# Optimization experiments

Measured on AMD Instinct MI355X. Metric: run time of the kernel, lower is better.

Reference implementation:

```python
import jax, jax.numpy as jnp
import numpy as np

HEADS = 8
DIM_HEAD = 64
SCALE = DIM_HEAD ** -0.5
POS_DIM = 64


def _sincos_pe(H, W, dim, dtype):
    # matches build_2d_sincos_pos_embed: [1, dim, H, W]
    y = jnp.linspace(-1.0, 1.0, H)[:, None] * jnp.ones((1, W), jnp.float32)
    x = jnp.ones((H, 1), jnp.float32) * jnp.linspace(-1.0, 1.0, W)[None, :]
    omega = 1.0 / (10000.0 ** (jnp.arange(dim // 4, dtype=jnp.float32) / (dim // 4)))
    px = x[..., None] * omega  # [H, W, dim//4]
    py = y[..., None] * omega
    pe = jnp.concatenate([jnp.sin(px), jnp.cos(px), jnp.sin(py), jnp.cos(py)], axis=-1)
    return pe.transpose(2, 0, 1)[None].astype(dtype)


def _conv2d(x, w):
    return jax.lax.conv_general_dilated(
        x, w, (1, 1), 'SAME', dimension_numbers=('NCHW', 'OIHW', 'NCHW'))


def _sobel(d):
    kx = jnp.array([[1, 0, -1], [2, 0, -2], [1, 0, -1]], jnp.float32).reshape(1, 1, 3, 3)
    ky = jnp.array([[1, 2, 1], [0, 0, 0], [-1, -2, -1]], jnp.float32).reshape(1, 1, 3, 3)
    return _conv2d(d, kx), _conv2d(d, ky)


def setup_inputs() -> dict:
    key = jax.random.key(0)
    ks = jax.random.split(key, 8)
    B, C, H, W = 2, 256, 64, 64
    hid = HEADS * DIM_HEAD  # 512
    s = 0.02
    return {
        'x': jax.random.normal(ks[0], (B, C, H, W), jnp.float32),
        'dsm': jax.random.uniform(ks[1], (B, 1, H, W), jnp.float32),
        'wq': jax.random.normal(ks[2], (hid, C), jnp.float32) * s,
        'wkv': jax.random.normal(ks[3], (2 * hid, C + 1), jnp.float32) * s,
        'wout': jax.random.normal(ks[4], (C, hid), jnp.float32) * s,
        'bout': jnp.zeros((C,), jnp.float32),
        'w_hape': jax.random.normal(ks[5], (hid, POS_DIM + 3), jnp.float32) * s,
        'b_hape': jnp.zeros((hid,), jnp.float32),
        'w_alpha': jax.random.normal(ks[6], (1, 1, 3, 3), jnp.float32) * 0.1,
        'b_alpha': jnp.zeros((1,), jnp.float32),
    }


def reference(x, dsm, wq, wkv, wout, bout, w_hape, b_hape, w_alpha, b_alpha):
    B, C, H, W = x.shape
    hid = wq.shape[0]
    # per-sample min-max normalize DSM over spatial dims
    dmin = dsm.min(axis=(2, 3), keepdims=True)
    dmax = dsm.max(axis=(2, 3), keepdims=True)
    d = (dsm - dmin) / (dmax - dmin + 1e-6)
    # HAPE: [PE | h | grad_h] -> 1x1 conv to hidden
    pe = jnp.broadcast_to(_sincos_pe(H, W, POS_DIM, x.dtype), (B, POS_DIM, H, W))
    gx, gy = _sobel(d)
    hape_in = jnp.concatenate([pe, d, gx, gy], axis=1)  # [B, 67, H, W]
    hape_k = jnp.einsum('oc,bchw->bohw', w_hape, hape_in) + b_hape[None, :, None, None]
    # QKV via 1x1 convs
    q = jnp.einsum('oc,bchw->bohw', wq, x)
    kv = jnp.einsum('oc,bchw->bohw', wkv, jnp.concatenate([x, d], axis=1))
    k = kv[:, :hid] + hape_k
    v = kv[:, hid:]
    to_heads = lambda t: t.reshape(B, HEADS, DIM_HEAD, H * W)  # b (h c) x y -> b h c (xy)
    qh = to_heads(q) * SCALE
    kh = to_heads(k)
    vh = to_heads(v)
    sim = jnp.einsum('bhdi,bhdj->bhij', qh, kh)  # [B, h, N, N]
    attn = jax.nn.softmax(sim, axis=-1)
    out = jnp.einsum('bhij,bhdj->bhid', attn, vh)  # [B, h, N, d]
    # b h (x y) d -> b (h d) x y
    out = out.transpose(0, 1, 3, 2).reshape(B, HEADS * DIM_HEAD, H, W)
    out = jnp.einsum('oc,bchw->bohw', wout, out) + bout[None, :, None, None]
    # fine: gradient-magnitude alpha gating
    mag = jnp.sqrt(jnp.maximum(gx, 0.0) ** 2 + jnp.maximum(gy, 0.0) ** 2 + 1e-12)
    alpha = jax.nn.sigmoid(_conv2d(mag, w_alpha) + b_alpha[None, :, None, None])
    return x + out * alpha
```

## Files before the change

### kernel.cpp

```cpp
#include <hip/hip_runtime.h>
#include <math.h>

#define NPOS 4096
#define MTOT 8192
#define KP   352
#define HT 64
#define WT 64

typedef unsigned short ushortT;
typedef short v8s __attribute__((ext_vector_type(8)));
typedef float v4f __attribute__((ext_vector_type(4)));

static __device__ __forceinline__ ushortT bfr(float f) {
    union { float f; unsigned u; } v; v.f = f;
    return (ushortT)((v.u + 0x8000u) >> 16);
}
static __device__ __forceinline__ unsigned pack2bf(float a, float b) {
    union { float f; unsigned u; } ua, ub; ua.f = a; ub.f = b;
    return __builtin_amdgcn_perm(ub.u + 0x8000u, ua.u + 0x8000u, 0x07060302u);
}
static __device__ __forceinline__ unsigned pack2bf_t(float a, float b) {
    union { float f; unsigned u; } ua, ub; ua.f = a; ub.f = b;
    return __builtin_amdgcn_perm(ub.u, ua.u, 0x07060302u);
}
static __device__ __forceinline__ float fexp2(float x) {
#if __has_builtin(__builtin_amdgcn_exp2f)
    return __builtin_amdgcn_exp2f(x);
#else
    return exp2f(x);
#endif
}

__global__ void k_minmax(const float* __restrict__ dsm, float* __restrict__ mm) {
    int b = blockIdx.x;
    const float* p = dsm + (size_t)b * NPOS;
    float mn = 1e30f, mx = -1e30f;
    for (int i = threadIdx.x; i < NPOS; i += 256) {
        float v = p[i];
        mn = fminf(mn, v); mx = fmaxf(mx, v);
    }
    for (int off = 32; off; off >>= 1) {
        mn = fminf(mn, __shfl_xor(mn, off, 64));
        mx = fmaxf(mx, __shfl_xor(mx, off, 64));
    }
    __shared__ float smn[4], smx[4];
    int wid = threadIdx.x >> 6;
    if ((threadIdx.x & 63) == 0) { smn[wid] = mn; smx[wid] = mx; }
    __syncthreads();
    if (threadIdx.x == 0) {
        mn = fminf(fminf(smn[0], smn[1]), fminf(smn[2], smn[3]));
        mx = fmaxf(fmaxf(smx[0], smx[1]), fmaxf(smx[2], smx[3]));
        mm[b * 2 + 0] = mn; mm[b * 2 + 1] = mx;
    }
}

__global__ void k_prep(const float* __restrict__ dsm, const float* __restrict__ mm,
                       const float* __restrict__ walpha, const float* __restrict__ balpha,
                       ushortT* __restrict__ F, float* __restrict__ alpha) {
    int idx = blockIdx.x * 256 + threadIdx.x;
    int b = idx / NPOS, n = idx % NPOS;
    int hh = n / WT, ww = n % WT;
    float dmin = mm[b * 2], dmax = mm[b * 2 + 1];
    float inv = 1.0f / (dmax - dmin + 1e-6f);
    const float* dp = dsm + (size_t)b * NPOS;

    float dwin[5][5];
    #pragma unroll
    for (int dy = 0; dy < 5; dy++)
        #pragma unroll
        for (int dx = 0; dx < 5; dx++) {
            int y = hh + dy - 2, x = ww + dx - 2;
            float v = 0.0f;
            if (y >= 0 && y < HT && x >= 0 && x < WT) v = (dp[y * WT + x] - dmin) * inv;
            dwin[dy][dx] = v;
        }

    float gxc = 0.f, gyc = 0.f;
    float conv = 0.f;
    #pragma unroll
    for (int oy = 0; oy < 3; oy++)
        #pragma unroll
        for (int ox = 0; ox < 3; ox++) {
            int qy = hh + oy - 1, qx = ww + ox - 1;
            float m = 0.0f;
            if (qy >= 0 && qy < HT && qx >= 0 && qx < WT) {
                float gx = dwin[oy][ox] - dwin[oy][ox + 2]
                         + 2.f * dwin[oy + 1][ox] - 2.f * dwin[oy + 1][ox + 2]
                         + dwin[oy + 2][ox] - dwin[oy + 2][ox + 2];
                float gy = dwin[oy][ox] + 2.f * dwin[oy][ox + 1] + dwin[oy][ox + 2]
                         - dwin[oy + 2][ox] - 2.f * dwin[oy + 2][ox + 1] - dwin[oy + 2][ox + 2];
                if (oy == 1 && ox == 1) { gxc = gx; gyc = gy; }
                float rx = fmaxf(gx, 0.f), ry = fmaxf(gy, 0.f);
                m = sqrtf(rx * rx + ry * ry + 1e-12f);
            }
            conv += walpha[oy * 3 + ox] * m;
        }
    alpha[idx] = 1.f / (1.f + __expf(-(conv + balpha[0])));

    ushortT* fb = F + (size_t)idx * KP;
    fb[256] = bfr(dwin[2][2]);
    fb[257] = bfr(gxc);
    fb[258] = bfr(gyc);
    float xc = -1.f + 2.f * (float)ww / 63.f;
    float yc = -1.f + 2.f * (float)hh / 63.f;
    const float l2w = 13.287712379549449f;
    #pragma unroll
    for (int i = 0; i < 16; i++) {
        float omega = exp2f(-(float)i * (l2w / 16.f));
        float px = xc * omega, py = yc * omega;
        fb[259 + i]      = bfr(__sinf(px));
        fb[259 + 16 + i] = bfr(__cosf(px));
        fb[259 + 32 + i] = bfr(__sinf(py));
        fb[259 + 48 + i] = bfr(__cosf(py));
    }
    #pragma unroll
    for (int z = 323; z < KP; z++) fb[z] = 0;
}

__global__ void k_cast(const float* __restrict__ x, ushortT* __restrict__ F) {
    __shared__ __align__(16) ushortT Tl[64][72];
    int nt = blockIdx.x * 64;
    int b = blockIdx.y >> 2, ct = (blockIdx.y & 3) * 64;
    int t = threadIdx.x;
    #pragma unroll
    for (int rep = 0; rep < 4; rep++) {
        int row = rep * 16 + (t >> 4), c4 = (t & 15) * 4;
        float4 f4 = *(const float4*)&x[((size_t)(b * 256 + ct + row)) * NPOS + nt + c4];
        Tl[c4 + 0][row] = bfr(f4.x);
        Tl[c4 + 1][row] = bfr(f4.y);
        Tl[c4 + 2][row] = bfr(f4.z);
        Tl[c4 + 3][row] = bfr(f4.w);
    }
    __syncthreads();
    #pragma unroll
    for (int rep = 0; rep < 2; rep++) {
        int slot = rep * 256 + t, row = slot >> 3, c8 = slot & 7;
        *(uint4*)&F[((size_t)(b * 4096 + nt + row)) * KP + ct + c8 * 8] = *(uint4*)&Tl[row][c8 * 8];
    }
}

__global__ void k_wcprep(const float* __restrict__ wq, const float* __restrict__ wkv,
                         const float* __restrict__ whape, const float* __restrict__ bhape,
                         ushortT* __restrict__ Wc, float* __restrict__ biasc) {
    int idx = blockIdx.x * 256 + threadIdx.x;
    int o = idx / KP, k = idx % KP;
    float v = 0.f;
    if (o < 512) {
        if (k < 256) v = wq[o * 256 + k] * 0.18033688011112042f;
        if (k == 0) biasc[o] = 0.f;
    } else if (o < 1024) {
        int r = o - 512;
        if (k < 257) v = wkv[r * 257 + k];
        if (k == 256)      v += whape[r * 67 + 64];
        else if (k == 257) v = whape[r * 67 + 65];
        else if (k == 258) v = whape[r * 67 + 66];
        else if (k >= 259 && k < 323) v = whape[r * 67 + (k - 259)];
        if (k == 0) biasc[o] = bhape[r];
    } else {
        int r = o - 512;
        if (k < 257) v = wkv[r * 257 + k];
        if (k == 0) biasc[o] = 0.f;
    }
    Wc[idx] = bfr(v);
}

__global__ void k_wout(const float* __restrict__ wout, ushortT* __restrict__ woutb) {
    int idx = blockIdx.x * 256 + threadIdx.x;
    woutb[idx] = bfr(wout[idx]);
}

__global__ __launch_bounds__(256) void k_gemm1(const ushortT* __restrict__ Wc, const ushortT* __restrict__ F,
                                               const float* __restrict__ biasc,
                                               ushortT* __restrict__ qT, ushortT* __restrict__ kT,
                                               ushortT* __restrict__ vv) {
    __shared__ __align__(16) ushortT Al[64][40];
    __shared__ __align__(16) ushortT Bl[64][40];
    __shared__ __align__(16) ushortT Vt[64][72];
    int mt = blockIdx.x * 64;
    int ot = blockIdx.y * 64;
    int t = threadIdx.x, w = t >> 6, lane = t & 63, u = lane & 15, quad = lane >> 4;
    int arow = t >> 2, ac8 = t & 3;
    v4f acc[4] = {};
    for (int k0 = 0; k0 < KP; k0 += 32) {
        __syncthreads();
        *(uint4*)&Al[arow][ac8 * 8] = *(const uint4*)&Wc[(size_t)(ot + arow) * KP + k0 + ac8 * 8];
        *(uint4*)&Bl[arow][ac8 * 8] = *(const uint4*)&F[(size_t)(mt + arow) * KP + k0 + ac8 * 8];
        __syncthreads();
        v8s a = *(v8s*)&Al[w * 16 + u][quad * 8];
        #pragma unroll
        for (int n4 = 0; n4 < 4; n4++) {
            v8s bb = *(v8s*)&Bl[n4 * 16 + u][quad * 8];
            acc[n4] = __builtin_amdgcn_mfma_f32_16x16x32_bf16(a, bb, acc[n4], 0, 0, 0);
        }
    }
    int obase = ot + w * 16 + quad * 4;
    float bo[4];
    #pragma unroll
    for (int r = 0; r < 4; r++) bo[r] = biasc[obase + r];
    if (ot < 1024) {
        int h = (ot >> 6) & 7;
        ushortT* dst = (ot < 512) ? qT : kT;
        #pragma unroll
        for (int n4 = 0; n4 < 4; n4++) {
            int m = mt + n4 * 16 + u;
            uint2 val;
            val.x = pack2bf(acc[n4][0] + bo[0], acc[n4][1] + bo[1]);
            val.y = pack2bf(acc[n4][2] + bo[2], acc[n4][3] + bo[3]);
            *(uint2*)&dst[((size_t)h * MTOT + m) * 64 + w * 16 + quad * 4] = val;
        }
    } else {
        __syncthreads();
        #pragma unroll
        for (int n4 = 0; n4 < 4; n4++) {
            int ml = n4 * 16 + u;
            #pragma unroll
            for (int r = 0; r < 4; r++) Vt[w * 16 + quad * 4 + r][ml] = bfr(acc[n4][r] + bo[r]);
        }
        __syncthreads();
        #pragma unroll
        for (int rep = 0; rep < 2; rep++) {
            int slot = rep * 256 + t, row = slot >> 3, c8 = slot & 7;
            *(uint4*)&vv[(size_t)(ot - 1024 + row) * MTOT + mt + c8 * 8] = *(uint4*)&Vt[row][c8 * 8];
        }
    }
}

#define LIDX(row, cb) (((row) << 6) + ((((cb) ^ ((row) & 7))) << 3))
__global__ __launch_bounds__(256, 2) void k_flash(const ushortT* __restrict__ qT,
                                                  const ushortT* __restrict__ kT,
                                                  const ushortT* __restrict__ vv,
                                                  float* __restrict__ Opart,
                                                  float* __restrict__ liPart) {
    __shared__ __align__(16) ushortT Kbuf[2][64 * 64];
    __shared__ __align__(16) ushortT Vbuf[2][64 * 64];
    __shared__ __align__(16) ushortT Pw[4][64 * 64];

    int it = blockIdx.x;
    int bh = blockIdx.y;
    int half = blockIdx.z;
    int b = bh >> 3, h = bh & 7;
    int colbase = b * NPOS;
    int t = threadIdx.x, w = t >> 6, lane = t & 63, u = lane & 15, quad = lane >> 4;
    int qb = it * 256 + w * 64;

    const ushortT* Qg = qT + ((size_t)h * MTOT + colbase + qb) * 64;
    const ushortT* Kg = kT + ((size_t)h * MTOT + colbase + half * 2048) * 64;
    const ushortT* Vg = vv + ((size_t)(h * 64)) * MTOT + colbase + half * 2048;
    ushortT* P = &Pw[w][0];

    int row0 = t >> 3,        c80 = t & 7;
    int row1 = (256 + t) >> 3, c81 = t & 7;

    v8s bq[4][2];
    #pragma unroll
    for (int g = 0; g < 4; g++)
        #pragma unroll
        for (int hf = 0; hf < 2; hf++)
            bq[g][hf] = *(const v8s*)&Qg[(size_t)(g * 16 + u) * 64 + hf * 32 + quad * 8];

    float li[4] = {0.f, 0.f, 0.f, 0.f};
    v4f O[4][4] = {};

    uint4 kr0 = *(const uint4*)&Kg[(size_t)row0 * 64 + c80 * 8];
    uint4 kr1 = *(const uint4*)&Kg[(size_t)row1 * 64 + c81 * 8];
    uint4 vr0 = *(const uint4*)&Vg[(size_t)row0 * MTOT + c80 * 8];
    uint4 vr1 = *(const uint4*)&Vg[(size_t)row1 * MTOT + c81 * 8];

    for (int jc = 0; jc < 32; jc++) {
        int cur = jc & 1;
        *(uint4*)&Kbuf[cur][LIDX(row0, c80)] = kr0;
        *(uint4*)&Kbuf[cur][LIDX(row1, c81)] = kr1;
        *(uint4*)&Vbuf[cur][LIDX(row0, c80)] = vr0;
        *(uint4*)&Vbuf[cur][LIDX(row1, c81)] = vr1;
        if (jc + 1 < 32) {
            int jb = (jc + 1) * 64;
            kr0 = *(const uint4*)&Kg[(size_t)(jb + row0) * 64 + c80 * 8];
            kr1 = *(const uint4*)&Kg[(size_t)(jb + row1) * 64 + c81 * 8];
            vr0 = *(const uint4*)&Vg[(size_t)row0 * MTOT + jb + c80 * 8];
            vr1 = *(const uint4*)&Vg[(size_t)row1 * MTOT + jb + c81 * 8];
        }
        __syncthreads();

        const ushortT* Kb = &Kbuf[cur][0];
        const ushortT* Vb = &Vbuf[cur][0];

        #pragma unroll
        for (int k4 = 0; k4 < 4; k4++) {
            v8s ak0 = *(const v8s*)&Kb[LIDX(k4 * 16 + u, quad)];
            v8s ak1 = *(const v8s*)&Kb[LIDX(k4 * 16 + u, 4 + quad)];
            v4f st[4];
            #pragma unroll
            for (int g = 0; g < 4; g++) {
                st[g] = (v4f){0.f, 0.f, 0.f, 0.f};
                st[g] = __builtin_amdgcn_mfma_f32_16x16x32_bf16(ak0, bq[g][0], st[g], 0, 0, 0);
                st[g] = __builtin_amdgcn_mfma_f32_16x16x32_bf16(ak1, bq[g][1], st[g], 0, 0, 0);
            }
            #pragma unroll
            for (int g = 0; g < 4; g++) {
                float p0 = fexp2(st[g][0]);
                float p1 = fexp2(st[g][1]);
                float p2 = fexp2(st[g][2]);
                float p3 = fexp2(st[g][3]);
                li[g] += (p0 + p1) + (p2 + p3);
                uint2 pv; pv.x = pack2bf_t(p0, p1); pv.y = pack2bf_t(p2, p3);
                *(uint2*)&P[LIDX(g * 16 + u, k4 * 2 + (quad >> 1)) + (quad & 1) * 4] = pv;
            }
        }

        v8s bp[4][2];
        #pragma unroll
        for (int g = 0; g < 4; g++)
            #pragma unroll
            for (int ks = 0; ks < 2; ks++)
                bp[g][ks] = *(v8s*)&P[LIDX(g * 16 + u, ks * 4 + quad)];
        #pragma unroll
        for (int d4 = 0; d4 < 4; d4++) {
            v8s av0 = *(const v8s*)&Vb[LIDX(d4 * 16 + u, quad)];
            v8s av1 = *(const v8s*)&Vb[LIDX(d4 * 16 + u, 4 + quad)];
            #pragma unroll
            for (int g = 0; g < 4; g++) {
                O[d4][g] = __builtin_amdgcn_mfma_f32_16x16x32_bf16(av0, bp[g][0], O[d4][g], 0, 0, 0);
                O[d4][g] = __builtin_amdgcn_mfma_f32_16x16x32_bf16(av1, bp[g][1], O[d4][g], 0, 0, 0);
            }
        }
    }

    #pragma unroll
    for (int g = 0; g < 4; g++) {
        li[g] += __shfl_xor(li[g], 16, 64);
        li[g] += __shfl_xor(li[g], 32, 64);
        int q = qb + g * 16 + u;
        size_t m2 = (size_t)(half * 2 + b) * 4096 + q;
        size_t base = m2 * 512 + h * 64;
        #pragma unroll
        for (int d4 = 0; d4 < 4; d4++) {
            float4 o4;
            o4.x = O[d4][g][0]; o4.y = O[d4][g][1]; o4.z = O[d4][g][2]; o4.w = O[d4][g][3];
            *(float4*)&Opart[base + d4 * 16 + quad * 4] = o4;
        }
        if (quad == 0) liPart[m2 * 8 + h] = li[g];
    }
}

__global__ __launch_bounds__(256) void k_comb(const float* __restrict__ Opart,
                                              const float* __restrict__ liPart,
                                              ushortT* __restrict__ aoB) {
    int tid = blockIdx.x * 256 + threadIdx.x;
    int m = tid >> 7, c4 = (tid & 127) * 4, h = c4 >> 6;
    float l = liPart[(size_t)m * 8 + h] + liPart[(size_t)(8192 + m) * 8 + h];
    float inv = 1.f / l;
    float4 o0 = *(const float4*)&Opart[(size_t)m * 512 + c4];
    float4 o1 = *(const float4*)&Opart[(size_t)(8192 + m) * 512 + c4];
    uint2 val;
    val.x = pack2bf((o0.x + o1.x) * inv, (o0.y + o1.y) * inv);
    val.y = pack2bf((o0.z + o1.z) * inv, (o0.w + o1.w) * inv);
    *(uint2*)&aoB[(size_t)m * 512 + c4] = val;
}

__global__ __launch_bounds__(256) void k_gemm2(const ushortT* __restrict__ woutb, const ushortT* __restrict__ aoB,
                                               const float* __restrict__ bout, const float* __restrict__ x,
                                               const float* __restrict__ alpha, float* __restrict__ out) {
    __shared__ __align__(16) ushortT Al[64][40];
    __shared__ __align__(16) ushortT Bl[64][40];
    int mt = blockIdx.x * 64;
    int ot = blockIdx.y * 64;
    int t = threadIdx.x, w = t >> 6, lane = t & 63, u = lane & 15, quad = lane >> 4;
    int arow = t >> 2, ac8 = t & 3;
    v4f acc[4] = {};
    for (int k0 = 0; k0 < 512; k0 += 32) {
        __syncthreads();
        *(uint4*)&Al[arow][ac8 * 8] = *(const uint4*)&woutb[(size_t)(ot + arow) * 512 + k0 + ac8 * 8];
        *(uint4*)&Bl[arow][ac8 * 8] = *(const uint4*)&aoB[(size_t)(mt + arow) * 512 + k0 + ac8 * 8];
        __syncthreads();
        v8s a = *(v8s*)&Al[w * 16 + u][quad * 8];
        #pragma unroll
        for (int n4 = 0; n4 < 4; n4++) {
            v8s bb = *(v8s*)&Bl[n4 * 16 + u][quad * 8];
            acc[n4] = __builtin_amdgcn_mfma_f32_16x16x32_bf16(a, bb, acc[n4], 0, 0, 0);
        }
    }
    int b = mt >> 12, n0 = mt & 4095;
    int obase = ot + w * 16 + quad * 4;
    float bo[4];
    #pragma unroll
    for (int r = 0; r < 4; r++) bo[r] = bout[obase + r];
    #pragma unroll
    for (int n4 = 0; n4 < 4; n4++) {
        int n = n0 + n4 * 16 + u;
        float al = alpha[(size_t)b * NPOS + n];
        #pragma unroll
        for (int r = 0; r < 4; r++) {
            size_t xi = ((size_t)(b * 256 + obase + r)) * NPOS + n;
            out[xi] = x[xi] + (acc[n4][r] + bo[r]) * al;
        }
    }
}

extern "C" void kernel_launch(void* const* d_in, const int* in_sizes, int n_in,
                              void* d_out, int out_size, void* d_ws, size_t ws_size,
                              hipStream_t stream) {
    const float* x      = (const float*)d_in[0];
    const float* dsm    = (const float*)d_in[1];
    const float* wq     = (const float*)d_in[2];
    const float* wkv    = (const float*)d_in[3];
    const float* wout   = (const float*)d_in[4];
    const float* bout   = (const float*)d_in[5];
    const float* whape  = (const float*)d_in[6];
    const float* bhape  = (const float*)d_in[7];
    const float* walpha = (const float*)d_in[8];
    const float* balpha = (const float*)d_in[9];
    float* out = (float*)d_out;
    float* ws  = (float*)d_ws;

    size_t off = 0;
    float* mm    = ws + off; off += 256;
    float* alpha = ws + off; off += (size_t)2 * NPOS;
    float* biasc = ws + off; off += 2048;
    float* Opart  = ws + off; off += (size_t)2 * MTOT * 512;
    float* liPart = ws + off; off += (size_t)2 * MTOT * 8;
    ushortT* F     = (ushortT*)(ws + off); off += (size_t)MTOT * KP / 2;
    ushortT* Wc    = (ushortT*)(ws + off); off += (size_t)1536 * KP / 2;
    ushortT* woutb = (ushortT*)(ws + off); off += (size_t)256 * 512 / 2;
    ushortT* qT    = (ushortT*)(ws + off); off += (size_t)8 * MTOT * 64 / 2;
    ushortT* kT    = (ushortT*)(ws + off); off += (size_t)8 * MTOT * 64 / 2;
    ushortT* vv    = (ushortT*)(ws + off); off += (size_t)512 * MTOT / 2;
    ushortT* aoB   = (ushortT*)(ws + off); off += (size_t)MTOT * 512 / 2;
    (void)in_sizes; (void)n_in; (void)out_size; (void)ws_size;

    k_minmax<<<2, 256, 0, stream>>>(dsm, mm);
    k_prep<<<32, 256, 0, stream>>>(dsm, mm, walpha, balpha, F, alpha);
    k_cast<<<dim3(64, 8), 256, 0, stream>>>(x, F);
    k_wcprep<<<(1536 * KP) / 256, 256, 0, stream>>>(wq, wkv, whape, bhape, Wc, biasc);
    k_wout<<<512, 256, 0, stream>>>(wout, woutb);
    k_gemm1<<<dim3(128, 24), 256, 0, stream>>>(Wc, F, biasc, qT, kT, vv);
    k_flash<<<dim3(16, 16, 2), 256, 0, stream>>>(qT, kT, vv, Opart, liPart);
    k_comb<<<4096, 256, 0, stream>>>(Opart, liPart, aoB);
    k_gemm2<<<dim3(128, 4), 256, 0, stream>>>(woutb, aoB, bout, x, alpha, out);
}
```

Measured before the change: 214.3 us.

## Shuffle P via permlane swaps, drop LDS staging, split keys four ways

The P tile (exp scores) is no longer written to and re-read from shared memory. It is packed in registers and moved into the MFMA B-operand layout with permlane32/permlane16 swap instructions. Removing the P buffer halves the kernel's shared memory, so launch bounds are raised to 4 blocks per CU, and the key range is split four ways instead of two to launch more blocks. The combine kernel now sums four partials, which doubles the fp32 partial-output traffic, and the tighter register budget at higher occupancy risks spills.

```diff
diff --git a/kernel.cpp b/kernel.cpp
--- a/kernel.cpp
+++ b/kernel.cpp
@@ -6,10 +6,14 @@
 #define KP   352
 #define HT 64
 #define WT 64
+#define NSPLIT 4
+#define KEYS_PER (NPOS / NSPLIT)
+#define NCH (KEYS_PER / 64)
 
 typedef unsigned short ushortT;
 typedef short v8s __attribute__((ext_vector_type(8)));
 typedef float v4f __attribute__((ext_vector_type(4)));
+typedef unsigned uint2v __attribute__((ext_vector_type(2)));
 
 static __device__ __forceinline__ ushortT bfr(float f) {
     union { float f; unsigned u; } v; v.f = f;
@@ -226,14 +230,13 @@
 }
 
 #define LIDX(row, cb) (((row) << 6) + ((((cb) ^ ((row) & 7))) << 3))
-__global__ __launch_bounds__(256, 2) void k_flash(const ushortT* __restrict__ qT,
+__global__ __launch_bounds__(256, 4) void k_flash(const ushortT* __restrict__ qT,
                                                   const ushortT* __restrict__ kT,
                                                   const ushortT* __restrict__ vv,
                                                   float* __restrict__ Opart,
                                                   float* __restrict__ liPart) {
     __shared__ __align__(16) ushortT Kbuf[2][64 * 64];
     __shared__ __align__(16) ushortT Vbuf[2][64 * 64];
-    __shared__ __align__(16) ushortT Pw[4][64 * 64];
 
     int it = blockIdx.x;
     int bh = blockIdx.y;
@@ -244,9 +247,8 @@
     int qb = it * 256 + w * 64;
 
     const ushortT* Qg = qT + ((size_t)h * MTOT + colbase + qb) * 64;
-    const ushortT* Kg = kT + ((size_t)h * MTOT + colbase + half * 2048) * 64;
-    const ushortT* Vg = vv + ((size_t)(h * 64)) * MTOT + colbase + half * 2048;
-    ushortT* P = &Pw[w][0];
+    const ushortT* Kg = kT + ((size_t)h * MTOT + colbase + half * KEYS_PER) * 64;
+    const ushortT* Vg = vv + ((size_t)(h * 64)) * MTOT + colbase + half * KEYS_PER;
 
     int row0 = t >> 3,        c80 = t & 7;
     int row1 = (256 + t) >> 3, c81 = t & 7;
@@ -266,13 +268,13 @@
     uint4 vr0 = *(const uint4*)&Vg[(size_t)row0 * MTOT + c80 * 8];
     uint4 vr1 = *(const uint4*)&Vg[(size_t)row1 * MTOT + c81 * 8];
 
-    for (int jc = 0; jc < 32; jc++) {
+    for (int jc = 0; jc < NCH; jc++) {
         int cur = jc & 1;
         *(uint4*)&Kbuf[cur][LIDX(row0, c80)] = kr0;
         *(uint4*)&Kbuf[cur][LIDX(row1, c81)] = kr1;
         *(uint4*)&Vbuf[cur][LIDX(row0, c80)] = vr0;
         *(uint4*)&Vbuf[cur][LIDX(row1, c81)] = vr1;
-        if (jc + 1 < 32) {
+        if (jc + 1 < NCH) {
             int jb = (jc + 1) * 64;
             kr0 = *(const uint4*)&Kg[(size_t)(jb + row0) * 64 + c80 * 8];
             kr1 = *(const uint4*)&Kg[(size_t)(jb + row1) * 64 + c81 * 8];
@@ -284,6 +286,7 @@
         const ushortT* Kb = &Kbuf[cur][0];
         const ushortT* Vb = &Vbuf[cur][0];
 
+        unsigned pk0[4][4], pk1[4][4];
         #pragma unroll
         for (int k4 = 0; k4 < 4; k4++) {
             v8s ak0 = *(const v8s*)&Kb[LIDX(k4 * 16 + u, quad)];
@@ -302,17 +305,26 @@
                 float p2 = fexp2(st[g][2]);
                 float p3 = fexp2(st[g][3]);
                 li[g] += (p0 + p1) + (p2 + p3);
-                uint2 pv; pv.x = pack2bf_t(p0, p1); pv.y = pack2bf_t(p2, p3);
-                *(uint2*)&P[LIDX(g * 16 + u, k4 * 2 + (quad >> 1)) + (quad & 1) * 4] = pv;
+                pk0[g][k4] = pack2bf_t(p0, p1);
+                pk1[g][k4] = pack2bf_t(p2, p3);
             }
         }
 
         v8s bp[4][2];
         #pragma unroll
-        for (int g = 0; g < 4; g++)
+        for (int g = 0; g < 4; g++) {
             #pragma unroll
-            for (int ks = 0; ks < 2; ks++)
-                bp[g][ks] = *(v8s*)&P[LIDX(g * 16 + u, ks * 4 + quad)];
+            for (int ks = 0; ks < 2; ks++) {
+                uint2v r0 = __builtin_amdgcn_permlane32_swap(pk0[g][2 * ks], pk0[g][2 * ks + 1], false, false);
+                uint2v r1 = __builtin_amdgcn_permlane32_swap(pk1[g][2 * ks], pk1[g][2 * ks + 1], false, false);
+                uint2v t0 = __builtin_amdgcn_permlane16_swap(r0.x, r0.y, false, false);
+                uint2v t1 = __builtin_amdgcn_permlane16_swap(r1.x, r1.y, false, false);
+                union { uint4 u4; v8s s; } cv;
+                cv.u4.x = t0.x; cv.u4.y = t1.x; cv.u4.z = t0.y; cv.u4.w = t1.y;
+                bp[g][ks] = cv.s;
+            }
+        }
+
         #pragma unroll
         for (int d4 = 0; d4 < 4; d4++) {
             v8s av0 = *(const v8s*)&Vb[LIDX(d4 * 16 + u, quad)];
@@ -347,13 +359,19 @@
                                               ushortT* __restrict__ aoB) {
     int tid = blockIdx.x * 256 + threadIdx.x;
     int m = tid >> 7, c4 = (tid & 127) * 4, h = c4 >> 6;
-    float l = liPart[(size_t)m * 8 + h] + liPart[(size_t)(8192 + m) * 8 + h];
+    float l = 0.f;
+    #pragma unroll
+    for (int s = 0; s < NSPLIT; s++) l += liPart[((size_t)s * 8192 + m) * 8 + h];
     float inv = 1.f / l;
-    float4 o0 = *(const float4*)&Opart[(size_t)m * 512 + c4];
-    float4 o1 = *(const float4*)&Opart[(size_t)(8192 + m) * 512 + c4];
+    float ox = 0.f, oy = 0.f, oz = 0.f, ow = 0.f;
+    #pragma unroll
+    for (int s = 0; s < NSPLIT; s++) {
+        float4 o = *(const float4*)&Opart[((size_t)s * 8192 + m) * 512 + c4];
+        ox += o.x; oy += o.y; oz += o.z; ow += o.w;
+    }
     uint2 val;
-    val.x = pack2bf((o0.x + o1.x) * inv, (o0.y + o1.y) * inv);
-    val.y = pack2bf((o0.z + o1.z) * inv, (o0.w + o1.w) * inv);
+    val.x = pack2bf(ox * inv, oy * inv);
+    val.y = pack2bf(oz * inv, ow * inv);
     *(uint2*)&aoB[(size_t)m * 512 + c4] = val;
 }
 
@@ -416,8 +434,8 @@
     float* mm    = ws + off; off += 256;
     float* alpha = ws + off; off += (size_t)2 * NPOS;
     float* biasc = ws + off; off += 2048;
-    float* Opart  = ws + off; off += (size_t)2 * MTOT * 512;
-    float* liPart = ws + off; off += (size_t)2 * MTOT * 8;
+    float* Opart  = ws + off; off += (size_t)NSPLIT * MTOT * 512;
+    float* liPart = ws + off; off += (size_t)NSPLIT * MTOT * 8;
     ushortT* F     = (ushortT*)(ws + off); off += (size_t)MTOT * KP / 2;
     ushortT* Wc    = (ushortT*)(ws + off); off += (size_t)1536 * KP / 2;
     ushortT* woutb = (ushortT*)(ws + off); off += (size_t)256 * 512 / 2;
@@ -433,7 +451,7 @@
     k_wcprep<<<(1536 * KP) / 256, 256, 0, stream>>>(wq, wkv, whape, bhape, Wc, biasc);
     k_wout<<<512, 256, 0, stream>>>(wout, woutb);
     k_gemm1<<<dim3(128, 24), 256, 0, stream>>>(Wc, F, biasc, qT, kT, vv);
-    k_flash<<<dim3(16, 16, 2), 256, 0, stream>>>(qT, kT, vv, Opart, liPart);
+    k_flash<<<dim3(16, 16, NSPLIT), 256, 0, stream>>>(qT, kT, vv, Opart, liPart);
     k_comb<<<4096, 256, 0, stream>>>(Opart, liPart, aoB);
     k_gemm2<<<dim3(128, 4), 256, 0, stream>>>(woutb, aoB, bout, x, alpha, out);
 }
```

Measured after the change: 727.3 us. 3.39x slower.
